# Kernel tuning notes

Hardware: AMD Instinct MI355X
Metric: run time of the kernel (lower is better)

The kernel has to match this reference:

```python
import jax, jax.numpy as jnp
import numpy as np

Q_SIZE, K_SIZE, H = 256, 256, 128
N, n, m, D_V = 4, 512, 512, 256

def setup_inputs() -> dict:
    key = jax.random.key(0)
    k1, k2, k3, k4, k5, k6 = jax.random.split(key, 6)
    return {
        "query": jax.random.normal(k1, (N, n, Q_SIZE), dtype=jnp.float32),
        "key": jax.random.normal(k2, (N, m, K_SIZE), dtype=jnp.float32),
        "value": jax.random.normal(k3, (N, m, D_V), dtype=jnp.float32),
        "W_q": jax.random.normal(k4, (Q_SIZE, H), dtype=jnp.float32) / np.sqrt(Q_SIZE),
        "W_k": jax.random.normal(k5, (K_SIZE, H), dtype=jnp.float32) / np.sqrt(K_SIZE),
        "W_v": jax.random.normal(k6, (H,), dtype=jnp.float32) / np.sqrt(H),
    }

def reference(query, key, value, W_q, W_k, W_v):
    q = query @ W_q                      # (N, n, h)
    k = key @ W_k                        # (N, m, h)
    # broadcast additive scores: tanh((N,n,1,h) + (N,1,m,h)) reduced by W_v -> (N,n,m)
    feats = jnp.tanh(q[:, :, None, :] + k[:, None, :, :])
    scores = jnp.einsum('bnmh,h->bnm', feats, W_v)
    attn = jax.nn.softmax(scores, axis=-1)  # softmax over keys m
    return jnp.einsum('bnm,bmd->bnd', attn, value)
```

## Files before the change

### kernel.cpp

```cpp
#include <hip/hip_runtime.h>
#include <math.h>

#define NB   4
#define SEQN 512
#define SEQM 512
#define QS   256
#define HH   128
#define DV   256
#define BM   (NB * SEQM)

static constexpr float kPreScale = 2.8853900817779268f;
static constexpr float kLog2e    = 1.4426950408889634f;

#if __has_builtin(__builtin_amdgcn_exp2f)
__device__ __forceinline__ float fexp2(float x) { return __builtin_amdgcn_exp2f(x); }
#else
__device__ __forceinline__ float fexp2(float x) { return exp2f(x); }
#endif

#if __has_builtin(__builtin_amdgcn_rcpf)
__device__ __forceinline__ float frcp(float x) { return __builtin_amdgcn_rcpf(x); }
#else
__device__ __forceinline__ float frcp(float x) { return 1.0f / x; }
#endif

__global__ __launch_bounds__(512) void proj_kernel(
    const float* __restrict__ query, const float* __restrict__ key,
    const float* __restrict__ Wq, const float* __restrict__ Wk,
    const float* __restrict__ wv,
    float* __restrict__ qt, float* __restrict__ ktT) {
  const int t = threadIdx.x;
  const int half = (NB * SEQN) / 8;
  const bool isK = blockIdx.x >= half;
  const int rb   = isK ? (blockIdx.x - half) : blockIdx.x;
  const float* __restrict__ in = isK ? key : query;
  const float* __restrict__ W  = isK ? Wk  : Wq;
  const int row0 = rb * 8;

  const int j  = t & 127;
  const int r0 = __builtin_amdgcn_readfirstlane((t >> 7) * 2);

  const float* __restrict__ x0p = in + (size_t)(row0 + r0 + 0) * QS;
  const float* __restrict__ x1p = in + (size_t)(row0 + r0 + 1) * QS;

  float a0 = 0.f, a1 = 0.f;
  for (int k0 = 0; k0 < QS; k0 += 4) {
    const float w0 = W[(k0 + 0) * HH + j];
    const float w1 = W[(k0 + 1) * HH + j];
    const float w2 = W[(k0 + 2) * HH + j];
    const float w3 = W[(k0 + 3) * HH + j];
    const float4 x0 = *reinterpret_cast<const float4*>(x0p + k0);
    const float4 x1 = *reinterpret_cast<const float4*>(x1p + k0);
    a0 = fmaf(x0.x, w0, fmaf(x0.y, w1, fmaf(x0.z, w2, fmaf(x0.w, w3, a0))));
    a1 = fmaf(x1.x, w0, fmaf(x1.y, w1, fmaf(x1.z, w2, fmaf(x1.w, w3, a1))));
  }
  const float wvj = wv[j];
  float acc[2] = {a0, a1};
#pragma unroll
  for (int r = 0; r < 2; ++r) {
    const float e  = fexp2(acc[r] * kPreScale);
    const float rc = frcp(e + 1.0f);
    float A = fmaf(-2.0f, rc, 1.0f);
    A = fminf(fmaxf(A, -0.99999988f), 0.99999988f);
    const int grow = row0 + r0 + r;
    if (isK) {
      ktT[(((size_t)(j >> 3) * BM) + grow) * 8 + (j & 7)] = A;
    } else {
      qt[(size_t)grow * (2 * HH) + j]      = A;
      qt[(size_t)grow * (2 * HH) + HH + j] = wvj * A;
    }
  }
}

__global__ __launch_bounds__(1024) void fused_kernel(
    const float* __restrict__ qt, const float* __restrict__ ktT,
    const float* __restrict__ wv, const float* __restrict__ value,
    float* __restrict__ out) {
  __shared__ float sp[8][SEQM];
  __shared__ float pvbuf[4][8][DV];
  __shared__ float rsh[8];

  const int t  = threadIdx.x;
  const int b  = blockIdx.x >> 6;
  const int n0 = (blockIdx.x & 63) * 8;
  const int mslot = t & 255;
  const int m0 = 2 * mslot;
  const int g2 = __builtin_amdgcn_readfirstlane((t >> 8) * 2);

  const float* __restrict__ qb = qt + ((size_t)b * SEQN + n0 + g2) * (2 * HH);
  const float* __restrict__ kbase = ktT + ((size_t)b * SEQM + m0) * 8;

  float N00 = 0.f, N01 = 0.f, N10 = 0.f, N11 = 0.f;
  float D00 = 1.f, D01 = 1.f, D10 = 1.f, D11 = 1.f;

  float4 f0, f1, f2, f3;
  f0 = *reinterpret_cast<const float4*>(kbase + 0);
  f1 = *reinterpret_cast<const float4*>(kbase + 4);
  f2 = *reinterpret_cast<const float4*>(kbase + 8);
  f3 = *reinterpret_cast<const float4*>(kbase + 12);

  for (int c = 0; c < 16; ++c) {
    const int h0 = c * 8;
    float bA0[8], bA1[8];
    bA0[0] = f0.x; bA0[1] = f0.y; bA0[2] = f0.z; bA0[3] = f0.w;
    bA0[4] = f1.x; bA0[5] = f1.y; bA0[6] = f1.z; bA0[7] = f1.w;
    bA1[0] = f2.x; bA1[1] = f2.y; bA1[2] = f2.z; bA1[3] = f2.w;
    bA1[4] = f3.x; bA1[5] = f3.y; bA1[6] = f3.z; bA1[7] = f3.w;
    if (c + 1 < 16) {
      const float* nb = kbase + (size_t)(c + 1) * BM * 8;
      f0 = *reinterpret_cast<const float4*>(nb + 0);
      f1 = *reinterpret_cast<const float4*>(nb + 4);
      f2 = *reinterpret_cast<const float4*>(nb + 8);
      f3 = *reinterpret_cast<const float4*>(nb + 12);
    }
    const float4 wva = *reinterpret_cast<const float4*>(wv + h0);
    const float4 wvb = *reinterpret_cast<const float4*>(wv + h0 + 4);
    float u0[8], u1[8];
    u0[0] = wva.x * bA0[0]; u1[0] = wva.x * bA1[0];
    u0[1] = wva.y * bA0[1]; u1[1] = wva.y * bA1[1];
    u0[2] = wva.z * bA0[2]; u1[2] = wva.z * bA1[2];
    u0[3] = wva.w * bA0[3]; u1[3] = wva.w * bA1[3];
    u0[4] = wvb.x * bA0[4]; u1[4] = wvb.x * bA1[4];
    u0[5] = wvb.y * bA0[5]; u1[5] = wvb.y * bA1[5];
    u0[6] = wvb.z * bA0[6]; u1[6] = wvb.z * bA1[6];
    u0[7] = wvb.w * bA0[7]; u1[7] = wvb.w * bA1[7];
#pragma unroll
    for (int n = 0; n < 2; ++n) {
      const float* qr = qb + n * (2 * HH);
      const float4 a0 = *reinterpret_cast<const float4*>(qr + h0);
      const float4 a1 = *reinterpret_cast<const float4*>(qr + h0 + 4);
      const float4 v0 = *reinterpret_cast<const float4*>(qr + HH + h0);
      const float4 v1 = *reinterpret_cast<const float4*>(qr + HH + h0 + 4);
#pragma unroll
      for (int mm = 0; mm < 2; ++mm) {
        const float* bA = (mm == 0) ? bA0 : bA1;
        const float* uu = (mm == 0) ? u0 : u1;
        const float s0 = v0.x + uu[0], d0 = fmaf(a0.x, bA[0], 1.0f);
        const float s1 = v0.y + uu[1], d1 = fmaf(a0.y, bA[1], 1.0f);
        const float s2 = v0.z + uu[2], d2 = fmaf(a0.z, bA[2], 1.0f);
        const float s3 = v0.w + uu[3], d3 = fmaf(a0.w, bA[3], 1.0f);
        const float s4 = v1.x + uu[4], d4 = fmaf(a1.x, bA[4], 1.0f);
        const float s5 = v1.y + uu[5], d5 = fmaf(a1.y, bA[5], 1.0f);
        const float s6 = v1.z + uu[6], d6 = fmaf(a1.z, bA[6], 1.0f);
        const float s7 = v1.w + uu[7], d7 = fmaf(a1.w, bA[7], 1.0f);
        const float t01 = fmaf(s0, d1, s1 * d0), e01 = d0 * d1;
        const float t23 = fmaf(s2, d3, s3 * d2), e23 = d2 * d3;
        const float t45 = fmaf(s4, d5, s5 * d4), e45 = d4 * d5;
        const float t67 = fmaf(s6, d7, s7 * d6), e67 = d6 * d7;
        const float t03 = fmaf(t01, e23, t23 * e01), e03 = e01 * e23;
        const float t47 = fmaf(t45, e67, t67 * e45), e47 = e45 * e67;
        const float t07 = fmaf(t03, e47, t47 * e03), e07 = e03 * e47;
        if (n == 0 && mm == 0) { N00 = fmaf(N00, e07, t07 * D00); D00 *= e07; }
        if (n == 0 && mm == 1) { N01 = fmaf(N01, e07, t07 * D01); D01 *= e07; }
        if (n == 1 && mm == 0) { N10 = fmaf(N10, e07, t07 * D10); D10 *= e07; }
        if (n == 1 && mm == 1) { N11 = fmaf(N11, e07, t07 * D11); D11 *= e07; }
      }
    }
  }
  sp[g2 + 0][m0 + 0] = N00 * frcp(D00);
  sp[g2 + 0][m0 + 1] = N01 * frcp(D01);
  sp[g2 + 1][m0 + 0] = N10 * frcp(D10);
  sp[g2 + 1][m0 + 1] = N11 * frcp(D11);
  __syncthreads();

  const int wave = t >> 6;
  const int lane = t & 63;
  const int row  = wave >> 1;
  const int hf   = wave & 1;
  float v[8];
  float mx = -1e30f;
#pragma unroll
  for (int i = 0; i < 8; ++i) {
    v[i] = sp[row][lane + 64 * i];
    mx = fmaxf(mx, v[i]);
  }
#pragma unroll
  for (int off = 32; off > 0; off >>= 1) mx = fmaxf(mx, __shfl_xor(mx, off));
  float p[8];
  float sum = 0.f;
#pragma unroll
  for (int i = 0; i < 8; ++i) {
    p[i] = fexp2((v[i] - mx) * kLog2e);
    sum += p[i];
  }
#pragma unroll
  for (int off = 32; off > 0; off >>= 1) sum += __shfl_xor(sum, off);
  __syncthreads();
#pragma unroll
  for (int i = 4 * hf; i < 4 * hf + 4; ++i) sp[row][lane + 64 * i] = p[i];
  if (hf == 0 && lane == 0) rsh[row] = frcp(sum);
  __syncthreads();

  const float* __restrict__ vb = value + (size_t)b * SEQM * DV;
  const int dp = (t & 127) * 2;
  const int mg = t >> 7;
  float o[8][2];
#pragma unroll
  for (int n = 0; n < 8; ++n) { o[n][0] = 0.f; o[n][1] = 0.f; }
  const int mbeg = mg * 64;
  for (int mi = 0; mi < 64; mi += 4) {
    const int mq = mbeg + mi;
    const float2 w0 = *reinterpret_cast<const float2*>(vb + (size_t)(mq + 0) * DV + dp);
    const float2 w1 = *reinterpret_cast<const float2*>(vb + (size_t)(mq + 1) * DV + dp);
    const float2 w2 = *reinterpret_cast<const float2*>(vb + (size_t)(mq + 2) * DV + dp);
    const float2 w3 = *reinterpret_cast<const float2*>(vb + (size_t)(mq + 3) * DV + dp);
#pragma unroll
    for (int n = 0; n < 8; ++n) {
      const float4 p4 = *reinterpret_cast<const float4*>(&sp[n][mq]);
      o[n][0] = fmaf(p4.x, w0.x, fmaf(p4.y, w1.x, fmaf(p4.z, w2.x, fmaf(p4.w, w3.x, o[n][0]))));
      o[n][1] = fmaf(p4.x, w0.y, fmaf(p4.y, w1.y, fmaf(p4.z, w2.y, fmaf(p4.w, w3.y, o[n][1]))));
    }
  }
  if (mg >= 4) {
#pragma unroll
    for (int n = 0; n < 8; ++n)
      *reinterpret_cast<float2*>(&pvbuf[mg - 4][n][dp]) = make_float2(o[n][0], o[n][1]);
  }
  __syncthreads();
  if (mg < 4) {
#pragma unroll
    for (int n = 0; n < 8; ++n) {
      float2 prev = *reinterpret_cast<const float2*>(&pvbuf[mg][n][dp]);
      prev.x += o[n][0]; prev.y += o[n][1];
      *reinterpret_cast<float2*>(&pvbuf[mg][n][dp]) = prev;
    }
  }
  __syncthreads();

  {
    const int n = t >> 7;
    const int d = t & 127;
    const float rsn = rsh[n];
    float accA = 0.f, accB = 0.f;
#pragma unroll
    for (int g = 0; g < 4; ++g) {
      accA += pvbuf[g][n][d];
      accB += pvbuf[g][n][d + 128];
    }
    const size_t ob = ((size_t)b * SEQN + n0 + n) * DV;
    out[ob + d]       = accA * rsn;
    out[ob + d + 128] = accB * rsn;
  }
}

extern "C" void kernel_launch(void* const* d_in, const int* in_sizes, int n_in,
                              void* d_out, int out_size, void* d_ws, size_t ws_size,
                              hipStream_t stream) {
  const float* query = (const float*)d_in[0];
  const float* key   = (const float*)d_in[1];
  const float* value = (const float*)d_in[2];
  const float* W_q   = (const float*)d_in[3];
  const float* W_k   = (const float*)d_in[4];
  const float* W_v   = (const float*)d_in[5];
  float* out = (float*)d_out;

  float* qt  = (float*)d_out;
  float* ktT = (float*)d_ws;

  proj_kernel<<<2 * (NB * SEQN) / 8, 512, 0, stream>>>(query, key, W_q, W_k, W_v, qt, ktT);
  fused_kernel<<<NB * (SEQN / 8), 1024, 0, stream>>>(qt, ktT, W_v, value, out);
}
```

Baseline: 46.26 us.

## Halve fused block size, give each thread four query rows, interleave q layout

The fused kernel now runs 512 threads per block instead of 1024. Each thread covers four query rows instead of two, so each loaded key chunk is reused across more rows and half as many threads reload it. The q projection output is interleaved per 8-wide chunk (A then wv*A) so one thread reads a contiguous 16-float segment. The softmax now uses one wave per row, with one fewer barrier, and the PV reduction runs over four groups finished by group 0. The risks are higher register pressure from eight accumulator pairs and less parallelism for hiding latency with fewer threads per block.

```diff
diff --git a/kernel.cpp b/kernel.cpp
--- a/kernel.cpp
+++ b/kernel.cpp
@@ -28,7 +28,7 @@
     const float* __restrict__ query, const float* __restrict__ key,
     const float* __restrict__ Wq, const float* __restrict__ Wk,
     const float* __restrict__ wv,
-    float* __restrict__ qt, float* __restrict__ ktT) {
+    float* __restrict__ qc, float* __restrict__ ktT) {
   const int t = threadIdx.x;
   const int half = (NB * SEQN) / 8;
   const bool isK = blockIdx.x >= half;
@@ -66,18 +66,19 @@
     if (isK) {
       ktT[(((size_t)(j >> 3) * BM) + grow) * 8 + (j & 7)] = A;
     } else {
-      qt[(size_t)grow * (2 * HH) + j]      = A;
-      qt[(size_t)grow * (2 * HH) + HH + j] = wvj * A;
+      const size_t base = (size_t)grow * 256 + (size_t)(j >> 3) * 16 + (j & 7);
+      qc[base]     = A;
+      qc[base + 8] = wvj * A;
     }
   }
 }
 
-__global__ __launch_bounds__(1024) void fused_kernel(
-    const float* __restrict__ qt, const float* __restrict__ ktT,
+__global__ __launch_bounds__(512) void fused_kernel(
+    const float* __restrict__ qc, const float* __restrict__ ktT,
     const float* __restrict__ wv, const float* __restrict__ value,
     float* __restrict__ out) {
   __shared__ float sp[8][SEQM];
-  __shared__ float pvbuf[4][8][DV];
+  __shared__ float pvbuf[3][8][DV];
   __shared__ float rsh[8];
 
   const int t  = threadIdx.x;
@@ -85,22 +86,21 @@
   const int n0 = (blockIdx.x & 63) * 8;
   const int mslot = t & 255;
   const int m0 = 2 * mslot;
-  const int g2 = __builtin_amdgcn_readfirstlane((t >> 8) * 2);
-
-  const float* __restrict__ qb = qt + ((size_t)b * SEQN + n0 + g2) * (2 * HH);
+  const int ng4 = __builtin_amdgcn_readfirstlane((t >> 8) * 4);
+
+  const float* __restrict__ qb = qc + ((size_t)(b * SEQN + n0 + ng4)) * 256;
   const float* __restrict__ kbase = ktT + ((size_t)b * SEQM + m0) * 8;
 
-  float N00 = 0.f, N01 = 0.f, N10 = 0.f, N11 = 0.f;
-  float D00 = 1.f, D01 = 1.f, D10 = 1.f, D11 = 1.f;
-
-  float4 f0, f1, f2, f3;
-  f0 = *reinterpret_cast<const float4*>(kbase + 0);
-  f1 = *reinterpret_cast<const float4*>(kbase + 4);
-  f2 = *reinterpret_cast<const float4*>(kbase + 8);
-  f3 = *reinterpret_cast<const float4*>(kbase + 12);
+  float N[4][2], D[4][2];
+#pragma unroll
+  for (int n = 0; n < 4; ++n) { N[n][0] = 0.f; N[n][1] = 0.f; D[n][0] = 1.f; D[n][1] = 1.f; }
+
+  float4 f0 = *reinterpret_cast<const float4*>(kbase + 0);
+  float4 f1 = *reinterpret_cast<const float4*>(kbase + 4);
+  float4 f2 = *reinterpret_cast<const float4*>(kbase + 8);
+  float4 f3 = *reinterpret_cast<const float4*>(kbase + 12);
 
   for (int c = 0; c < 16; ++c) {
-    const int h0 = c * 8;
     float bA0[8], bA1[8];
     bA0[0] = f0.x; bA0[1] = f0.y; bA0[2] = f0.z; bA0[3] = f0.w;
     bA0[4] = f1.x; bA0[5] = f1.y; bA0[6] = f1.z; bA0[7] = f1.w;
@@ -113,8 +113,8 @@
       f2 = *reinterpret_cast<const float4*>(nb + 8);
       f3 = *reinterpret_cast<const float4*>(nb + 12);
     }
-    const float4 wva = *reinterpret_cast<const float4*>(wv + h0);
-    const float4 wvb = *reinterpret_cast<const float4*>(wv + h0 + 4);
+    const float4 wva = *reinterpret_cast<const float4*>(wv + c * 8);
+    const float4 wvb = *reinterpret_cast<const float4*>(wv + c * 8 + 4);
     float u0[8], u1[8];
     u0[0] = wva.x * bA0[0]; u1[0] = wva.x * bA1[0];
     u0[1] = wva.y * bA0[1]; u1[1] = wva.y * bA1[1];
@@ -125,24 +125,24 @@
     u0[6] = wvb.z * bA0[6]; u1[6] = wvb.z * bA1[6];
     u0[7] = wvb.w * bA0[7]; u1[7] = wvb.w * bA1[7];
 #pragma unroll
-    for (int n = 0; n < 2; ++n) {
-      const float* qr = qb + n * (2 * HH);
-      const float4 a0 = *reinterpret_cast<const float4*>(qr + h0);
-      const float4 a1 = *reinterpret_cast<const float4*>(qr + h0 + 4);
-      const float4 v0 = *reinterpret_cast<const float4*>(qr + HH + h0);
-      const float4 v1 = *reinterpret_cast<const float4*>(qr + HH + h0 + 4);
+    for (int n = 0; n < 4; ++n) {
+      const float* qr = qb + (size_t)n * 256 + (size_t)c * 16;
+      const float4 qa0 = *reinterpret_cast<const float4*>(qr + 0);
+      const float4 qa1 = *reinterpret_cast<const float4*>(qr + 4);
+      const float4 qv0 = *reinterpret_cast<const float4*>(qr + 8);
+      const float4 qv1 = *reinterpret_cast<const float4*>(qr + 12);
 #pragma unroll
       for (int mm = 0; mm < 2; ++mm) {
         const float* bA = (mm == 0) ? bA0 : bA1;
         const float* uu = (mm == 0) ? u0 : u1;
-        const float s0 = v0.x + uu[0], d0 = fmaf(a0.x, bA[0], 1.0f);
-        const float s1 = v0.y + uu[1], d1 = fmaf(a0.y, bA[1], 1.0f);
-        const float s2 = v0.z + uu[2], d2 = fmaf(a0.z, bA[2], 1.0f);
-        const float s3 = v0.w + uu[3], d3 = fmaf(a0.w, bA[3], 1.0f);
-        const float s4 = v1.x + uu[4], d4 = fmaf(a1.x, bA[4], 1.0f);
-        const float s5 = v1.y + uu[5], d5 = fmaf(a1.y, bA[5], 1.0f);
-        const float s6 = v1.z + uu[6], d6 = fmaf(a1.z, bA[6], 1.0f);
-        const float s7 = v1.w + uu[7], d7 = fmaf(a1.w, bA[7], 1.0f);
+        const float s0 = qv0.x + uu[0], d0 = fmaf(qa0.x, bA[0], 1.0f);
+        const float s1 = qv0.y + uu[1], d1 = fmaf(qa0.y, bA[1], 1.0f);
+        const float s2 = qv0.z + uu[2], d2 = fmaf(qa0.z, bA[2], 1.0f);
+        const float s3 = qv0.w + uu[3], d3 = fmaf(qa0.w, bA[3], 1.0f);
+        const float s4 = qv1.x + uu[4], d4 = fmaf(qa1.x, bA[4], 1.0f);
+        const float s5 = qv1.y + uu[5], d5 = fmaf(qa1.y, bA[5], 1.0f);
+        const float s6 = qv1.z + uu[6], d6 = fmaf(qa1.z, bA[6], 1.0f);
+        const float s7 = qv1.w + uu[7], d7 = fmaf(qa1.w, bA[7], 1.0f);
         const float t01 = fmaf(s0, d1, s1 * d0), e01 = d0 * d1;
         const float t23 = fmaf(s2, d3, s3 * d2), e23 = d2 * d3;
         const float t45 = fmaf(s4, d5, s5 * d4), e45 = d4 * d5;
@@ -150,45 +150,41 @@
         const float t03 = fmaf(t01, e23, t23 * e01), e03 = e01 * e23;
         const float t47 = fmaf(t45, e67, t67 * e45), e47 = e45 * e67;
         const float t07 = fmaf(t03, e47, t47 * e03), e07 = e03 * e47;
-        if (n == 0 && mm == 0) { N00 = fmaf(N00, e07, t07 * D00); D00 *= e07; }
-        if (n == 0 && mm == 1) { N01 = fmaf(N01, e07, t07 * D01); D01 *= e07; }
-        if (n == 1 && mm == 0) { N10 = fmaf(N10, e07, t07 * D10); D10 *= e07; }
-        if (n == 1 && mm == 1) { N11 = fmaf(N11, e07, t07 * D11); D11 *= e07; }
+        N[n][mm] = fmaf(N[n][mm], e07, t07 * D[n][mm]);
+        D[n][mm] *= e07;
       }
     }
   }
-  sp[g2 + 0][m0 + 0] = N00 * frcp(D00);
-  sp[g2 + 0][m0 + 1] = N01 * frcp(D01);
-  sp[g2 + 1][m0 + 0] = N10 * frcp(D10);
-  sp[g2 + 1][m0 + 1] = N11 * frcp(D11);
+#pragma unroll
+  for (int n = 0; n < 4; ++n) {
+    sp[ng4 + n][m0 + 0] = N[n][0] * frcp(D[n][0]);
+    sp[ng4 + n][m0 + 1] = N[n][1] * frcp(D[n][1]);
+  }
   __syncthreads();
 
   const int wave = t >> 6;
   const int lane = t & 63;
-  const int row  = wave >> 1;
-  const int hf   = wave & 1;
-  float v[8];
-  float mx = -1e30f;
-#pragma unroll
-  for (int i = 0; i < 8; ++i) {
-    v[i] = sp[row][lane + 64 * i];
-    mx = fmaxf(mx, v[i]);
-  }
-#pragma unroll
-  for (int off = 32; off > 0; off >>= 1) mx = fmaxf(mx, __shfl_xor(mx, off));
-  float p[8];
-  float sum = 0.f;
-#pragma unroll
-  for (int i = 0; i < 8; ++i) {
-    p[i] = fexp2((v[i] - mx) * kLog2e);
-    sum += p[i];
-  }
-#pragma unroll
-  for (int off = 32; off > 0; off >>= 1) sum += __shfl_xor(sum, off);
-  __syncthreads();
-#pragma unroll
-  for (int i = 4 * hf; i < 4 * hf + 4; ++i) sp[row][lane + 64 * i] = p[i];
-  if (hf == 0 && lane == 0) rsh[row] = frcp(sum);
+  {
+    float v[8];
+    float mx = -1e30f;
+#pragma unroll
+    for (int i = 0; i < 8; ++i) {
+      v[i] = sp[wave][lane + 64 * i];
+      mx = fmaxf(mx, v[i]);
+    }
+#pragma unroll
+    for (int off = 32; off > 0; off >>= 1) mx = fmaxf(mx, __shfl_xor(mx, off));
+    float sum = 0.f;
+#pragma unroll
+    for (int i = 0; i < 8; ++i) {
+      const float p = fexp2((v[i] - mx) * kLog2e);
+      sum += p;
+      sp[wave][lane + 64 * i] = p;
+    }
+#pragma unroll
+    for (int off = 32; off > 0; off >>= 1) sum += __shfl_xor(sum, off);
+    if (lane == 0) rsh[wave] = frcp(sum);
+  }
   __syncthreads();
 
   const float* __restrict__ vb = value + (size_t)b * SEQM * DV;
@@ -197,8 +193,8 @@
   float o[8][2];
 #pragma unroll
   for (int n = 0; n < 8; ++n) { o[n][0] = 0.f; o[n][1] = 0.f; }
-  const int mbeg = mg * 64;
-  for (int mi = 0; mi < 64; mi += 4) {
+  const int mbeg = mg * 128;
+  for (int mi = 0; mi < 128; mi += 4) {
     const int mq = mbeg + mi;
     const float2 w0 = *reinterpret_cast<const float2*>(vb + (size_t)(mq + 0) * DV + dp);
     const float2 w1 = *reinterpret_cast<const float2*>(vb + (size_t)(mq + 1) * DV + dp);
@@ -211,35 +207,26 @@
       o[n][1] = fmaf(p4.x, w0.y, fmaf(p4.y, w1.y, fmaf(p4.z, w2.y, fmaf(p4.w, w3.y, o[n][1]))));
     }
   }
-  if (mg >= 4) {
+  if (mg >= 1) {
 #pragma unroll
     for (int n = 0; n < 8; ++n)
-      *reinterpret_cast<float2*>(&pvbuf[mg - 4][n][dp]) = make_float2(o[n][0], o[n][1]);
+      *reinterpret_cast<float2*>(&pvbuf[mg - 1][n][dp]) = make_float2(o[n][0], o[n][1]);
   }
   __syncthreads();
-  if (mg < 4) {
+  if (mg == 0) {
 #pragma unroll
     for (int n = 0; n < 8; ++n) {
-      float2 prev = *reinterpret_cast<const float2*>(&pvbuf[mg][n][dp]);
-      prev.x += o[n][0]; prev.y += o[n][1];
-      *reinterpret_cast<float2*>(&pvbuf[mg][n][dp]) = prev;
-    }
-  }
-  __syncthreads();
-
-  {
-    const int n = t >> 7;
-    const int d = t & 127;
-    const float rsn = rsh[n];
-    float accA = 0.f, accB = 0.f;
-#pragma unroll
-    for (int g = 0; g < 4; ++g) {
-      accA += pvbuf[g][n][d];
-      accB += pvbuf[g][n][d + 128];
-    }
-    const size_t ob = ((size_t)b * SEQN + n0 + n) * DV;
-    out[ob + d]       = accA * rsn;
-    out[ob + d + 128] = accB * rsn;
+      const float rsn = rsh[n];
+      float accA = o[n][0], accB = o[n][1];
+#pragma unroll
+      for (int g = 0; g < 3; ++g) {
+        accA += pvbuf[g][n][dp];
+        accB += pvbuf[g][n][dp + 1];
+      }
+      const size_t ob = ((size_t)b * SEQN + n0 + n) * DV;
+      out[ob + dp]     = accA * rsn;
+      out[ob + dp + 1] = accB * rsn;
+    }
   }
 }
 
@@ -254,9 +241,9 @@
   const float* W_v   = (const float*)d_in[5];
   float* out = (float*)d_out;
 
-  float* qt  = (float*)d_out;
+  float* qc  = (float*)d_out;
   float* ktT = (float*)d_ws;
 
-  proj_kernel<<<2 * (NB * SEQN) / 8, 512, 0, stream>>>(query, key, W_q, W_k, W_v, qt, ktT);
-  fused_kernel<<<NB * (SEQN / 8), 1024, 0, stream>>>(qt, ktT, W_v, value, out);
+  proj_kernel<<<2 * (NB * SEQN) / 8, 512, 0, stream>>>(query, key, W_q, W_k, W_v, qc, ktT);
+  fused_kernel<<<NB * (SEQN / 8), 512, 0, stream>>>(qc, ktT, W_v, value, out);
 }
```

New measurement: 45.64 us. Within noise of the previous version (-1.3%).

## Compute tanh scores from exponentials with paired reciprocals instead of the tanh-addition formula

Applied to the files above, without the earlier changes.

The projection kernel now stores exp(2x) for q and k instead of tanh values, and no longer writes the W_v-scaled copy of q. The fused kernel uses tanh(q+k) = 1 - 2/(1+Eq*Ek). It drops the constant sum of W_v, which softmax ignores, and accumulates -2*sum w/(1+Eq*Ek), merging pairs of terms so each pair needs only one reciprocal. This replaces the running rational N/D accumulation and halves the q data read per row. In exchange it adds reciprocal instructions to the inner loop, removes the clamping, and could lose accuracy or overflow for large projections. q now goes to the workspace instead of the output buffer.

```diff
diff --git a/kernel.cpp b/kernel.cpp
--- a/kernel.cpp
+++ b/kernel.cpp
@@ -27,8 +27,7 @@
 __global__ __launch_bounds__(512) void proj_kernel(
     const float* __restrict__ query, const float* __restrict__ key,
     const float* __restrict__ Wq, const float* __restrict__ Wk,
-    const float* __restrict__ wv,
-    float* __restrict__ qt, float* __restrict__ ktT) {
+    float* __restrict__ qE, float* __restrict__ ktE) {
   const int t = threadIdx.x;
   const int half = (NB * SEQN) / 8;
   const bool isK = blockIdx.x >= half;
@@ -54,26 +53,21 @@
     a0 = fmaf(x0.x, w0, fmaf(x0.y, w1, fmaf(x0.z, w2, fmaf(x0.w, w3, a0))));
     a1 = fmaf(x1.x, w0, fmaf(x1.y, w1, fmaf(x1.z, w2, fmaf(x1.w, w3, a1))));
   }
-  const float wvj = wv[j];
   float acc[2] = {a0, a1};
 #pragma unroll
   for (int r = 0; r < 2; ++r) {
-    const float e  = fexp2(acc[r] * kPreScale);
-    const float rc = frcp(e + 1.0f);
-    float A = fmaf(-2.0f, rc, 1.0f);
-    A = fminf(fmaxf(A, -0.99999988f), 0.99999988f);
+    const float E = fexp2(acc[r] * kPreScale);
     const int grow = row0 + r0 + r;
     if (isK) {
-      ktT[(((size_t)(j >> 3) * BM) + grow) * 8 + (j & 7)] = A;
+      ktE[(((size_t)(j >> 3) * BM) + grow) * 8 + (j & 7)] = E;
     } else {
-      qt[(size_t)grow * (2 * HH) + j]      = A;
-      qt[(size_t)grow * (2 * HH) + HH + j] = wvj * A;
+      qE[(size_t)grow * HH + j] = E;
     }
   }
 }
 
 __global__ __launch_bounds__(1024) void fused_kernel(
-    const float* __restrict__ qt, const float* __restrict__ ktT,
+    const float* __restrict__ qE, const float* __restrict__ ktE,
     const float* __restrict__ wv, const float* __restrict__ value,
     float* __restrict__ out) {
   __shared__ float sp[8][SEQM];
@@ -87,25 +81,24 @@
   const int m0 = 2 * mslot;
   const int g2 = __builtin_amdgcn_readfirstlane((t >> 8) * 2);
 
-  const float* __restrict__ qb = qt + ((size_t)b * SEQN + n0 + g2) * (2 * HH);
-  const float* __restrict__ kbase = ktT + ((size_t)b * SEQM + m0) * 8;
-
-  float N00 = 0.f, N01 = 0.f, N10 = 0.f, N11 = 0.f;
-  float D00 = 1.f, D01 = 1.f, D10 = 1.f, D11 = 1.f;
-
-  float4 f0, f1, f2, f3;
-  f0 = *reinterpret_cast<const float4*>(kbase + 0);
-  f1 = *reinterpret_cast<const float4*>(kbase + 4);
-  f2 = *reinterpret_cast<const float4*>(kbase + 8);
-  f3 = *reinterpret_cast<const float4*>(kbase + 12);
+  const float* __restrict__ qb = qE + ((size_t)(b * SEQN + n0 + g2)) * HH;
+  const float* __restrict__ kbase = ktE + ((size_t)b * SEQM + m0) * 8;
+
+  float acc[2][2];
+  acc[0][0] = 0.f; acc[0][1] = 0.f; acc[1][0] = 0.f; acc[1][1] = 0.f;
+
+  float4 f0 = *reinterpret_cast<const float4*>(kbase + 0);
+  float4 f1 = *reinterpret_cast<const float4*>(kbase + 4);
+  float4 f2 = *reinterpret_cast<const float4*>(kbase + 8);
+  float4 f3 = *reinterpret_cast<const float4*>(kbase + 12);
 
   for (int c = 0; c < 16; ++c) {
     const int h0 = c * 8;
-    float bA0[8], bA1[8];
-    bA0[0] = f0.x; bA0[1] = f0.y; bA0[2] = f0.z; bA0[3] = f0.w;
-    bA0[4] = f1.x; bA0[5] = f1.y; bA0[6] = f1.z; bA0[7] = f1.w;
-    bA1[0] = f2.x; bA1[1] = f2.y; bA1[2] = f2.z; bA1[3] = f2.w;
-    bA1[4] = f3.x; bA1[5] = f3.y; bA1[6] = f3.z; bA1[7] = f3.w;
+    float k0a[8], k1a[8];
+    k0a[0] = f0.x; k0a[1] = f0.y; k0a[2] = f0.z; k0a[3] = f0.w;
+    k0a[4] = f1.x; k0a[5] = f1.y; k0a[6] = f1.z; k0a[7] = f1.w;
+    k1a[0] = f2.x; k1a[1] = f2.y; k1a[2] = f2.z; k1a[3] = f2.w;
+    k1a[4] = f3.x; k1a[5] = f3.y; k1a[6] = f3.z; k1a[7] = f3.w;
     if (c + 1 < 16) {
       const float* nb = kbase + (size_t)(c + 1) * BM * 8;
       f0 = *reinterpret_cast<const float4*>(nb + 0);
@@ -115,52 +108,41 @@
     }
     const float4 wva = *reinterpret_cast<const float4*>(wv + h0);
     const float4 wvb = *reinterpret_cast<const float4*>(wv + h0 + 4);
-    float u0[8], u1[8];
-    u0[0] = wva.x * bA0[0]; u1[0] = wva.x * bA1[0];
-    u0[1] = wva.y * bA0[1]; u1[1] = wva.y * bA1[1];
-    u0[2] = wva.z * bA0[2]; u1[2] = wva.z * bA1[2];
-    u0[3] = wva.w * bA0[3]; u1[3] = wva.w * bA1[3];
-    u0[4] = wvb.x * bA0[4]; u1[4] = wvb.x * bA1[4];
-    u0[5] = wvb.y * bA0[5]; u1[5] = wvb.y * bA1[5];
-    u0[6] = wvb.z * bA0[6]; u1[6] = wvb.z * bA1[6];
-    u0[7] = wvb.w * bA0[7]; u1[7] = wvb.w * bA1[7];
 #pragma unroll
     for (int n = 0; n < 2; ++n) {
-      const float* qr = qb + n * (2 * HH);
-      const float4 a0 = *reinterpret_cast<const float4*>(qr + h0);
-      const float4 a1 = *reinterpret_cast<const float4*>(qr + h0 + 4);
-      const float4 v0 = *reinterpret_cast<const float4*>(qr + HH + h0);
-      const float4 v1 = *reinterpret_cast<const float4*>(qr + HH + h0 + 4);
+      const float* qr = qb + n * HH;
+      const float4 qa = *reinterpret_cast<const float4*>(qr + h0);
+      const float4 qc4 = *reinterpret_cast<const float4*>(qr + h0 + 4);
+      const float Eq0 = qa.x,  Eq1 = qa.y,  Eq2 = qa.z,  Eq3 = qa.w;
+      const float Eq4 = qc4.x, Eq5 = qc4.y, Eq6 = qc4.z, Eq7 = qc4.w;
 #pragma unroll
       for (int mm = 0; mm < 2; ++mm) {
-        const float* bA = (mm == 0) ? bA0 : bA1;
-        const float* uu = (mm == 0) ? u0 : u1;
-        const float s0 = v0.x + uu[0], d0 = fmaf(a0.x, bA[0], 1.0f);
-        const float s1 = v0.y + uu[1], d1 = fmaf(a0.y, bA[1], 1.0f);
-        const float s2 = v0.z + uu[2], d2 = fmaf(a0.z, bA[2], 1.0f);
-        const float s3 = v0.w + uu[3], d3 = fmaf(a0.w, bA[3], 1.0f);
-        const float s4 = v1.x + uu[4], d4 = fmaf(a1.x, bA[4], 1.0f);
-        const float s5 = v1.y + uu[5], d5 = fmaf(a1.y, bA[5], 1.0f);
-        const float s6 = v1.z + uu[6], d6 = fmaf(a1.z, bA[6], 1.0f);
-        const float s7 = v1.w + uu[7], d7 = fmaf(a1.w, bA[7], 1.0f);
-        const float t01 = fmaf(s0, d1, s1 * d0), e01 = d0 * d1;
-        const float t23 = fmaf(s2, d3, s3 * d2), e23 = d2 * d3;
-        const float t45 = fmaf(s4, d5, s5 * d4), e45 = d4 * d5;
-        const float t67 = fmaf(s6, d7, s7 * d6), e67 = d6 * d7;
-        const float t03 = fmaf(t01, e23, t23 * e01), e03 = e01 * e23;
-        const float t47 = fmaf(t45, e67, t67 * e45), e47 = e45 * e67;
-        const float t07 = fmaf(t03, e47, t47 * e03), e07 = e03 * e47;
-        if (n == 0 && mm == 0) { N00 = fmaf(N00, e07, t07 * D00); D00 *= e07; }
-        if (n == 0 && mm == 1) { N01 = fmaf(N01, e07, t07 * D01); D01 *= e07; }
-        if (n == 1 && mm == 0) { N10 = fmaf(N10, e07, t07 * D10); D10 *= e07; }
-        if (n == 1 && mm == 1) { N11 = fmaf(N11, e07, t07 * D11); D11 *= e07; }
+        const float* Ek = (mm == 0) ? k0a : k1a;
+        const float d0 = fmaf(Eq0, Ek[0], 1.0f);
+        const float d1 = fmaf(Eq1, Ek[1], 1.0f);
+        const float d2 = fmaf(Eq2, Ek[2], 1.0f);
+        const float d3 = fmaf(Eq3, Ek[3], 1.0f);
+        const float d4 = fmaf(Eq4, Ek[4], 1.0f);
+        const float d5 = fmaf(Eq5, Ek[5], 1.0f);
+        const float d6 = fmaf(Eq6, Ek[6], 1.0f);
+        const float d7 = fmaf(Eq7, Ek[7], 1.0f);
+        const float n01 = fmaf(wva.x, d1, wva.y * d0);
+        const float n23 = fmaf(wva.z, d3, wva.w * d2);
+        const float n45 = fmaf(wvb.x, d5, wvb.y * d4);
+        const float n67 = fmaf(wvb.z, d7, wvb.w * d6);
+        float a = acc[n][mm];
+        a = fmaf(n01, frcp(d0 * d1), a);
+        a = fmaf(n23, frcp(d2 * d3), a);
+        a = fmaf(n45, frcp(d4 * d5), a);
+        a = fmaf(n67, frcp(d6 * d7), a);
+        acc[n][mm] = a;
       }
     }
   }
-  sp[g2 + 0][m0 + 0] = N00 * frcp(D00);
-  sp[g2 + 0][m0 + 1] = N01 * frcp(D01);
-  sp[g2 + 1][m0 + 0] = N10 * frcp(D10);
-  sp[g2 + 1][m0 + 1] = N11 * frcp(D11);
+  sp[g2 + 0][m0 + 0] = -2.0f * acc[0][0];
+  sp[g2 + 0][m0 + 1] = -2.0f * acc[0][1];
+  sp[g2 + 1][m0 + 0] = -2.0f * acc[1][0];
+  sp[g2 + 1][m0 + 1] = -2.0f * acc[1][1];
   __syncthreads();
 
   const int wave = t >> 6;
@@ -254,9 +236,9 @@
   const float* W_v   = (const float*)d_in[5];
   float* out = (float*)d_out;
 
-  float* qt  = (float*)d_out;
-  float* ktT = (float*)d_ws;
-
-  proj_kernel<<<2 * (NB * SEQN) / 8, 512, 0, stream>>>(query, key, W_q, W_k, W_v, qt, ktT);
-  fused_kernel<<<NB * (SEQN / 8), 1024, 0, stream>>>(qt, ktT, W_v, value, out);
+  float* ktE = (float*)d_ws;
+  float* qE  = ktE + (size_t)16 * BM * 8;
+
+  proj_kernel<<<2 * (NB * SEQN) / 8, 512, 0, stream>>>(query, key, W_q, W_k, qE, ktE);
+  fused_kernel<<<NB * (SEQN / 8), 1024, 0, stream>>>(qE, ktE, W_v, value, out);
 }
```

Result: no change. 45.71 us (-1.2%).
